# Kernel tuning notes

Measured on AMD Instinct MI355X. Metric: run time of the kernel, lower is better.

## Reference

```python
import jax, jax.numpy as jnp
import numpy as np

D_MODEL = 1024
D_STATE = 16
D_CONV = 4
EXPAND = 2
D_INNER = EXPAND * D_MODEL          # 2048
DT_RANK = D_INNER // 16             # 128
BATCH = 2
SEQLEN = 1024


def _silu(x):
    return x * jax.nn.sigmoid(x)


def setup_inputs() -> dict:
    key = jax.random.key(0)
    ks = jax.random.split(key, 8)
    s = 0.02
    A_init = jnp.tile(jnp.arange(1, D_STATE + 1, dtype=jnp.float32)[None, :], (D_INNER, 1))
    return {
        "x": jax.random.normal(ks[0], (BATCH, SEQLEN, D_MODEL), jnp.float32),
        "W_in": jax.random.normal(ks[1], (D_MODEL, 2 * D_INNER), jnp.float32) * s,
        "conv_k": jax.random.normal(ks[2], (D_CONV, 1, D_INNER), jnp.float32) * s,  # (kw, in/groups, out)
        "conv_b": jnp.zeros((D_INNER,), jnp.float32),
        "W_xproj": jax.random.normal(ks[3], (D_INNER, DT_RANK + 2 * D_STATE), jnp.float32) * s,
        "W_dt": jax.random.normal(ks[4], (DT_RANK, D_INNER), jnp.float32) * s,
        "b_dt": jnp.zeros((D_INNER,), jnp.float32),
        "A_log": jnp.log(A_init),
        "D": jnp.ones((D_INNER,), jnp.float32),
        "W_out": jax.random.normal(ks[5], (D_INNER, D_MODEL), jnp.float32) * s,
    }


def reference(x, W_in, conv_k, conv_b, W_xproj, W_dt, b_dt, A_log, D, W_out):
    # in_proj and gate split
    xz = x @ W_in                                   # (B, L, 2*Di)
    x_in, z = jnp.split(xz, 2, axis=-1)             # each (B, L, Di)

    # depthwise causal conv1d: left-pad by d_conv-1 (keras padding='causal')
    xp = jnp.pad(x_in, ((0, 0), (D_CONV - 1, 0), (0, 0)))
    x_in = jax.lax.conv_general_dilated(
        xp, conv_k, window_strides=(1,), padding='VALID',
        dimension_numbers=('NWC', 'WIO', 'NWC'),
        feature_group_count=D_INNER) + conv_b
    u = _silu(x_in)                                 # (B, L, Di)

    # input-dependent SSM params
    x_dbl = u @ W_xproj                             # (B, L, dt_rank + 2*N)
    dt_low, Bm, Cm = jnp.split(x_dbl, [DT_RANK, DT_RANK + D_STATE], axis=-1)
    dt = jax.nn.softplus(dt_low @ W_dt + b_dt)      # (B, L, Di)
    A = -jnp.exp(A_log)                             # (Di, N)
    dA = jnp.exp(jnp.einsum('bld,dn->bldn', dt, A)) # (B, L, Di, N)
    dB = jnp.einsum('bld,bln->bldn', dt, Bm)        # (B, L, Di, N)

    # selective scan over sequence length
    def step(h, e):
        a_t, b_t, u_t, c_t = e                      # (B,Di,N), (B,Di,N), (B,Di), (B,N)
        h = a_t * h + b_t * u_t[..., None]
        y_t = jnp.einsum('bdn,bn->bd', h, c_t)
        return h, y_t

    h0 = jnp.zeros((x.shape[0], D_INNER, D_STATE), dtype=x.dtype)
    xs = (jnp.swapaxes(dA, 0, 1), jnp.swapaxes(dB, 0, 1),
          jnp.swapaxes(u, 0, 1), jnp.swapaxes(Cm, 0, 1))
    _, yT = jax.lax.scan(step, h0, xs)              # (L, B, Di)
    y = jnp.swapaxes(yT, 0, 1) + u * D              # skip connection

    return (y * _silu(z)) @ W_out                   # (B, L, d_model)
```

## Files before the change

kernel.cpp:

```cpp
#include <hip/hip_runtime.h>
#include <hip/hip_bf16.h>

#define D_MODEL 1024
#define D_STATE 16
#define D_CONV 4
#define D_INNER 2048
#define DT_RANK 128
#define BATCH 2
#define SEQLEN 1024
#define XCOLS 160
#define NCHUNK 32
#define LCHUNK 32

typedef __hip_bfloat16 bf16;
typedef __attribute__((ext_vector_type(8))) short short8;
typedef __attribute__((ext_vector_type(4))) float f32x4;

__device__ __forceinline__ unsigned short f2bf_bits(float f) {
    bf16 h = __float2bfloat16(f);
    return *(unsigned short*)&h;
}

__device__ __forceinline__ float softplus_f(float x) {
    return fmaxf(x, 0.f) + __logf(1.f + __expf(-fabsf(x)));
}

__device__ __forceinline__ float silu_f(float x) {
    return x / (1.f + __expf(-x));
}

__device__ __forceinline__ void load16_lds(void* lds, const void* g) {
    __builtin_amdgcn_global_load_lds(
        (const __attribute__((address_space(1))) unsigned int*)g,
        (__attribute__((address_space(3))) unsigned int*)lds, 16, 0, 0);
}

__device__ __forceinline__ void transpose_tile(const float* __restrict__ B,
                                               bf16* __restrict__ Bt,
                                               int K, int N, int nt, int kt,
                                               float (*t)[33], int tid)
{
    const int tx = tid & 31, ty = tid >> 5;
    const int n0 = nt * 32, k0 = kt * 32;
    #pragma unroll
    for (int r = 0; r < 4; ++r) {
        int n = n0 + tx;
        t[ty + r * 8][tx] = (n < N) ? B[(size_t)(k0 + ty + r * 8) * N + n] : 0.f;
    }
    __syncthreads();
    #pragma unroll
    for (int r = 0; r < 4; ++r)
        Bt[(size_t)(n0 + ty + r * 8) * K + k0 + tx] = __float2bfloat16(t[tx][ty + r * 8]);
}

__global__ __launch_bounds__(256)
void prep_kernel(const float* __restrict__ x, bf16* __restrict__ x_bf,
                 const float* __restrict__ W_in, bf16* __restrict__ Win_t,
                 const float* __restrict__ W_xproj, bf16* __restrict__ Wxp_t,
                 const float* __restrict__ W_dt, bf16* __restrict__ Wdt_t,
                 const float* __restrict__ W_out, bf16* __restrict__ Wout_t,
                 const float* __restrict__ A_log, float* __restrict__ Aneg)
{
    __shared__ float t[32][33];
    const int tid = threadIdx.x;
    int blk = blockIdx.x;
    if (blk < 4096) {
        transpose_tile(W_in, Win_t, D_MODEL, 2 * D_INNER, blk & 127, blk >> 7, t, tid);
        return;
    }
    blk -= 4096;
    if (blk < 512) {
        transpose_tile(W_xproj, Wxp_t, D_INNER, XCOLS, blk & 7, blk >> 3, t, tid);
        return;
    }
    blk -= 512;
    if (blk < 256) {
        transpose_tile(W_dt, Wdt_t, DT_RANK, D_INNER, blk & 63, blk >> 6, t, tid);
        return;
    }
    blk -= 256;
    if (blk < 2048) {
        transpose_tile(W_out, Wout_t, D_INNER, D_MODEL, blk & 31, blk >> 5, t, tid);
        return;
    }
    blk -= 2048;
    if (blk < 2048) {
        int i = blk * 256 + tid;
        float4 v = ((const float4*)x)[i];
        ushort4 p;
        p.x = f2bf_bits(v.x); p.y = f2bf_bits(v.y);
        p.z = f2bf_bits(v.z); p.w = f2bf_bits(v.w);
        ((ushort4*)x_bf)[i] = p;
        return;
    }
    blk -= 2048;
    {
        int i = blk * 256 + tid;
        Aneg[i] = -__expf(A_log[i]);
    }
}

template<int BN, int EPI>
__global__ __launch_bounds__(256)
void gemm_mfma(const bf16* __restrict__ A, const bf16* __restrict__ Bt,
               float* __restrict__ C, bf16* __restrict__ Cb,
               const float* __restrict__ bias,
               int M, int N, int K, int ldc, int kchunk)
{
    constexpr int WN = (BN == 128) ? 64 : 32;
    constexpr int NJ = WN / 16;
    __shared__ short As[128 * 32];
    __shared__ short Bs[BN * 32];
    const int tid = threadIdx.x;
    const int lane = tid & 63, wave = tid >> 6;
    const int wm = (wave >> 1) * 64, wn = (wave & 1) * WN;
    const int row0 = blockIdx.y * 128, col0 = blockIdx.x * BN;
    const int r_m = lane & 15, r_q = lane >> 4;
    const int kstart = blockIdx.z * kchunk;
    float* Cz = C + (size_t)blockIdx.z * M * ldc;

    const int srow = tid >> 2, schk = (tid & 3) * 8;
    const bf16* Ag0 = A  + (size_t)(row0 + srow)      * K + kstart + schk;
    const bf16* Ag1 = A  + (size_t)(row0 + srow + 64) * K + kstart + schk;
    const bf16* Bg0 = Bt + (size_t)(col0 + srow)      * K + kstart + schk;
    const bf16* Bg1 = Bt + (size_t)(col0 + srow + 64) * K + kstart + schk;
    short* AsW0 = &As[8 * tid];
    short* AsW1 = &As[8 * tid + 2048];
    short* BsW0 = &Bs[8 * tid];
    short* BsW1 = &Bs[8 * tid + 2048];

    f32x4 acc[4][NJ];
    #pragma unroll
    for (int i = 0; i < 4; ++i)
        #pragma unroll
        for (int j = 0; j < NJ; ++j)
            #pragma unroll
            for (int r = 0; r < 4; ++r) acc[i][j][r] = 0.f;

    for (int k0 = 0; k0 < kchunk; k0 += 32) {
        __syncthreads();
        load16_lds(AsW0, Ag0 + k0);
        load16_lds(AsW1, Ag1 + k0);
        load16_lds(BsW0, Bg0 + k0);
        if (BN == 128) load16_lds(BsW1, Bg1 + k0);
        __syncthreads();
        short8 af[4], bfr[NJ];
        #pragma unroll
        for (int i = 0; i < 4; ++i)
            af[i] = *(const short8*)&As[(wm + i * 16 + r_m) * 32 + r_q * 8];
        #pragma unroll
        for (int j = 0; j < NJ; ++j)
            bfr[j] = *(const short8*)&Bs[(wn + j * 16 + r_m) * 32 + r_q * 8];
        #pragma unroll
        for (int i = 0; i < 4; ++i)
            #pragma unroll
            for (int j = 0; j < NJ; ++j)
                acc[i][j] = __builtin_amdgcn_mfma_f32_16x16x32_bf16(
                    af[i], bfr[j], acc[i][j], 0, 0, 0);
    }

    #pragma unroll
    for (int i = 0; i < 4; ++i) {
        #pragma unroll
        for (int j = 0; j < NJ; ++j) {
            int row = row0 + wm + i * 16 + r_q * 4;
            int col = col0 + wn + j * 16 + r_m;
            if (col < N) {
                if (EPI == 1) {
                    float bv = bias[col];
                    #pragma unroll
                    for (int r = 0; r < 4; ++r)
                        Cb[(size_t)(row + r) * ldc + col] =
                            __float2bfloat16(softplus_f(acc[i][j][r] + bv));
                } else if (EPI == 2) {
                    if (col < 2048) {
                        #pragma unroll
                        for (int r = 0; r < 4; ++r)
                            Cz[(size_t)(row + r) * ldc + col] = acc[i][j][r];
                    } else {
                        int zc = col - 2048;
                        #pragma unroll
                        for (int r = 0; r < 4; ++r)
                            Cb[(size_t)(row + r) * ldc + zc] =
                                __float2bfloat16(silu_f(acc[i][j][r]));
                    }
                } else {
                    #pragma unroll
                    for (int r = 0; r < 4; ++r)
                        Cz[(size_t)(row + r) * ldc + col] = acc[i][j][r];
                }
            }
        }
    }
}

__global__ __launch_bounds__(256)
void reduce_xdbl(const float* __restrict__ Cpart, float* __restrict__ x_dbl,
                 bf16* __restrict__ dtA_bf)
{
    int i = blockIdx.x * 256 + threadIdx.x;
    if (i >= 2048 * XCOLS) return;
    int r = i / XCOLS, c = i - r * XCOLS;
    float s = 0.f;
    #pragma unroll
    for (int z = 0; z < 8; ++z)
        s += Cpart[(size_t)z * 2048 * 256 + (size_t)r * 256 + c];
    x_dbl[i] = s;
    if (c < DT_RANK) dtA_bf[(size_t)r * DT_RANK + c] = __float2bfloat16(s);
}

__global__ __launch_bounds__(256)
void reduce_out(const float* __restrict__ Cpart, float* __restrict__ out)
{
    int i = blockIdx.x * 256 + threadIdx.x;
    const size_t stride = (size_t)2048 * 1024 / 4;
    const float4* p = (const float4*)Cpart;
    float4 a = p[i], b = p[i + stride], c = p[i + 2 * stride], d = p[i + 3 * stride];
    float4 r;
    r.x = (a.x + b.x) + (c.x + d.x);
    r.y = (a.y + b.y) + (c.y + d.y);
    r.z = (a.z + b.z) + (c.z + d.z);
    r.w = (a.w + b.w) + (c.w + d.w);
    ((float4*)out)[i] = r;
}

__global__ __launch_bounds__(256)
void conv_silu_kernel(const float* __restrict__ x_lin,
                      const float* __restrict__ conv_k,
                      const float* __restrict__ conv_b,
                      bf16* __restrict__ u_bf)
{
    int idx4 = blockIdx.x * 256 + threadIdx.x;
    int d4 = idx4 & (D_INNER / 4 - 1);
    int t = (idx4 >> 9) & (SEQLEN - 1);
    int b = idx4 >> 19;
    float4 acc = ((const float4*)conv_b)[d4];
    #pragma unroll
    for (int k = 0; k < D_CONV; ++k) {
        int tt = t + k - (D_CONV - 1);
        if (tt >= 0) {
            float4 xv = ((const float4*)x_lin)[(size_t)(b * SEQLEN + tt) * (D_INNER / 4) + d4];
            float4 kv = ((const float4*)conv_k)[k * (D_INNER / 4) + d4];
            acc.x = fmaf(xv.x, kv.x, acc.x);
            acc.y = fmaf(xv.y, kv.y, acc.y);
            acc.z = fmaf(xv.z, kv.z, acc.z);
            acc.w = fmaf(xv.w, kv.w, acc.w);
        }
    }
    ushort4 pk;
    pk.x = f2bf_bits(acc.x / (1.f + __expf(-acc.x)));
    pk.y = f2bf_bits(acc.y / (1.f + __expf(-acc.y)));
    pk.z = f2bf_bits(acc.z / (1.f + __expf(-acc.z)));
    pk.w = f2bf_bits(acc.w / (1.f + __expf(-acc.w)));
    ((ushort4*)u_bf)[idx4] = pk;
}

__global__ __launch_bounds__(256)
void scan_phase1(const bf16* __restrict__ dt_sb,
                 const float* __restrict__ Aneg,
                 const bf16* __restrict__ u_bf,
                 const float* __restrict__ x_dbl,
                 float* __restrict__ Pst, float* __restrict__ Sst)
{
    __shared__ float Bsm[LCHUNK][16];
    const int d = blockIdx.x * 256 + threadIdx.x;
    const int c = blockIdx.y, b = blockIdx.z;
    const int t0 = c * LCHUNK;
    for (int i = threadIdx.x; i < LCHUNK * 16; i += 256) {
        int tt = i >> 4, n = i & 15;
        Bsm[tt][n] = x_dbl[(size_t)(b * SEQLEN + t0 + tt) * XCOLS + DT_RANK + n];
    }
    float A_row[D_STATE];
    const float4* a4 = (const float4*)(Aneg + d * D_STATE);
    #pragma unroll
    for (int q = 0; q < 4; ++q) {
        float4 v = a4[q];
        A_row[q*4+0] = v.x; A_row[q*4+1] = v.y; A_row[q*4+2] = v.z; A_row[q*4+3] = v.w;
    }
    __syncthreads();
    float P[D_STATE], S[D_STATE];
    #pragma unroll
    for (int n = 0; n < D_STATE; ++n) { P[n] = 1.f; S[n] = 0.f; }
    const bf16* dpp = dt_sb + (size_t)(b * SEQLEN + t0) * D_INNER + d;
    const bf16* upp = u_bf + (size_t)(b * SEQLEN + t0) * D_INNER + d;
    #pragma unroll 8
    for (int t = 0; t < LCHUNK; ++t) {
        float dtv = __bfloat162float(dpp[(size_t)t * D_INNER]);
        float du = dtv * __bfloat162float(upp[(size_t)t * D_INNER]);
        const float4* b4 = (const float4*)&Bsm[t][0];
        #pragma unroll
        for (int q = 0; q < 4; ++q) {
            float4 v = b4[q];
            float Bn[4] = {v.x, v.y, v.z, v.w};
            #pragma unroll
            for (int e = 0; e < 4; ++e) {
                int n = q * 4 + e;
                float a = __expf(dtv * A_row[n]);
                P[n] *= a;
                S[n] = fmaf(a, S[n], du * Bn[e]);
            }
        }
    }
    const size_t base = ((size_t)(b * NCHUNK + c) * D_STATE) * D_INNER + d;
    #pragma unroll
    for (int n = 0; n < D_STATE; ++n) {
        Pst[base + (size_t)n * D_INNER] = P[n];
        Sst[base + (size_t)n * D_INNER] = S[n];
    }
}

__global__ __launch_bounds__(256)
void scan_phase2(const float* __restrict__ Pst, float* __restrict__ Sst)
{
    const int d = blockIdx.x * 256 + threadIdx.x;
    const int n = blockIdx.y;
    const int b = blockIdx.z;
    float h = 0.f;
    for (int c = 0; c < NCHUNK; ++c) {
        const size_t idx = ((size_t)(b * NCHUNK + c) * D_STATE + n) * D_INNER + d;
        float Pv = Pst[idx], Sv = Sst[idx];
        Sst[idx] = h;
        h = fmaf(Pv, h, Sv);
    }
}

__global__ __launch_bounds__(256)
void scan_phase3(const bf16* __restrict__ dt_sb,
                 const float* __restrict__ Aneg,
                 const bf16* __restrict__ u_bf,
                 const float* __restrict__ x_dbl,
                 const float* __restrict__ Dvec,
                 const bf16* __restrict__ sz_bf,
                 const float* __restrict__ hin,
                 bf16* __restrict__ g_bf)
{
    __shared__ float BCs[LCHUNK][32];
    const int d = blockIdx.x * 256 + threadIdx.x;
    const int c = blockIdx.y, b = blockIdx.z;
    const int t0 = c * LCHUNK;
    for (int i = threadIdx.x; i < LCHUNK * 32; i += 256) {
        int tt = i >> 5, col = i & 31;
        BCs[tt][col] = x_dbl[(size_t)(b * SEQLEN + t0 + tt) * XCOLS + DT_RANK + col];
    }
    float A_row[D_STATE];
    const float4* a4 = (const float4*)(Aneg + d * D_STATE);
    #pragma unroll
    for (int q = 0; q < 4; ++q) {
        float4 v = a4[q];
        A_row[q*4+0] = v.x; A_row[q*4+1] = v.y; A_row[q*4+2] = v.z; A_row[q*4+3] = v.w;
    }
    const float Dd = Dvec[d];
    __syncthreads();
    float h[D_STATE];
    const size_t base = ((size_t)(b * NCHUNK + c) * D_STATE) * D_INNER + d;
    #pragma unroll
    for (int n = 0; n < D_STATE; ++n) h[n] = hin[base + (size_t)n * D_INNER];
    const bf16* dpp = dt_sb + (size_t)(b * SEQLEN + t0) * D_INNER + d;
    const bf16* upp = u_bf + (size_t)(b * SEQLEN + t0) * D_INNER + d;
    const bf16* zpp = sz_bf + (size_t)(b * SEQLEN + t0) * D_INNER + d;
    bf16* gpp = g_bf + (size_t)(b * SEQLEN + t0) * D_INNER + d;
    #pragma unroll 8
    for (int t = 0; t < LCHUNK; ++t) {
        float dtv = __bfloat162float(dpp[(size_t)t * D_INNER]);
        float uv = __bfloat162float(upp[(size_t)t * D_INNER]);
        float sz = __bfloat162float(zpp[(size_t)t * D_INNER]);
        float du = dtv * uv;
        float y = 0.f;
        const float4* bc4 = (const float4*)&BCs[t][0];
        #pragma unroll
        for (int q = 0; q < 4; ++q) {
            float4 v = bc4[q];
            float4 w = bc4[q + 4];
            float Bn[4] = {v.x, v.y, v.z, v.w};
            float Cn[4] = {w.x, w.y, w.z, w.w};
            #pragma unroll
            for (int e = 0; e < 4; ++e) {
                int n = q * 4 + e;
                float a = __expf(dtv * A_row[n]);
                h[n] = fmaf(a, h[n], du * Bn[e]);
                y = fmaf(h[n], Cn[e], y);
            }
        }
        float gy = y + uv * Dd;
        gpp[(size_t)t * D_INNER] = __float2bfloat16(gy * sz);
    }
}

extern "C" void kernel_launch(void* const* d_in, const int* in_sizes, int n_in,
                              void* d_out, int out_size, void* d_ws, size_t ws_size,
                              hipStream_t stream)
{
    const float* x      = (const float*)d_in[0];
    const float* W_in   = (const float*)d_in[1];
    const float* conv_k = (const float*)d_in[2];
    const float* conv_b = (const float*)d_in[3];
    const float* W_xproj= (const float*)d_in[4];
    const float* W_dt   = (const float*)d_in[5];
    const float* b_dt   = (const float*)d_in[6];
    const float* A_log  = (const float*)d_in[7];
    const float* Dvec   = (const float*)d_in[8];
    const float* W_out  = (const float*)d_in[9];
    float* out = (float*)d_out;

    const int BL = BATCH * SEQLEN;

    float* ws     = (float*)d_ws;
    float* x_lin  = ws;
    float* x_dbl  = x_lin + (size_t)BL * D_INNER;
    float* Pst    = x_dbl + (size_t)BL * XCOLS;
    float* Sst    = Pst + (size_t)BATCH * NCHUNK * D_STATE * D_INNER;
    float* Aneg   = Sst + (size_t)BATCH * NCHUNK * D_STATE * D_INNER;
    float* Cpart  = Aneg + 32768;
    bf16*  x_bf   = (bf16*)Cpart;
    bf16* Win_t  = (bf16*)(Cpart + (size_t)4 * 2048 * 1024);
    bf16* u_bf   = Win_t + (size_t)4096 * 1024;
    bf16* sz_bf  = u_bf  + (size_t)BL * D_INNER;
    bf16* Wxp_t  = sz_bf + (size_t)BL * D_INNER;
    bf16* dtA_bf = Wxp_t + (size_t)256 * 2048;
    bf16* Wdt_t  = dtA_bf+ (size_t)BL * DT_RANK;
    bf16* g_bf   = Wdt_t + (size_t)2048 * 128;
    bf16* Wout_t = g_bf  + (size_t)BL * D_INNER;
    bf16* dt_sb  = Wout_t+ (size_t)1024 * 2048;

    prep_kernel<<<4096 + 512 + 256 + 2048 + 2048 + 128, 256, 0, stream>>>(
        x, x_bf, W_in, Win_t, W_xproj, Wxp_t, W_dt, Wdt_t, W_out, Wout_t, A_log, Aneg);

    gemm_mfma<128, 2><<<dim3(32, 16, 1), 256, 0, stream>>>(
        x_bf, Win_t, x_lin, sz_bf, nullptr, BL, 2 * D_INNER, D_MODEL, D_INNER, D_MODEL);

    conv_silu_kernel<<<(BL * D_INNER / 4) / 256, 256, 0, stream>>>(x_lin, conv_k, conv_b, u_bf);

    gemm_mfma<64, 0><<<dim3(3, 16, 8), 256, 0, stream>>>(
        u_bf, Wxp_t, Cpart, nullptr, nullptr, BL, 256, D_INNER, 256, 256);
    reduce_xdbl<<<(BL * XCOLS + 255) / 256, 256, 0, stream>>>(Cpart, x_dbl, dtA_bf);

    gemm_mfma<64, 1><<<dim3(32, 16, 1), 256, 0, stream>>>(
        dtA_bf, Wdt_t, nullptr, dt_sb, b_dt, BL, D_INNER, DT_RANK, D_INNER, DT_RANK);

    scan_phase1<<<dim3(D_INNER / 256, NCHUNK, BATCH), 256, 0, stream>>>(
        dt_sb, Aneg, u_bf, x_dbl, Pst, Sst);
    scan_phase2<<<dim3(D_INNER / 256, D_STATE, BATCH), 256, 0, stream>>>(Pst, Sst);
    scan_phase3<<<dim3(D_INNER / 256, NCHUNK, BATCH), 256, 0, stream>>>(
        dt_sb, Aneg, u_bf, x_dbl, Dvec, sz_bf, Sst, g_bf);

    gemm_mfma<128, 0><<<dim3(8, 16, 4), 256, 0, stream>>>(
        g_bf, Wout_t, Cpart, nullptr, nullptr, BL, D_MODEL, D_INNER, D_MODEL, D_INNER / 4);
    reduce_out<<<(BL * D_MODEL / 4) / 256, 256, 0, stream>>>(Cpart, out);
}
```

Before: 255.7 us.

## Store in-proj x as bf16, vectorize conv and reductions, retile out-proj split-K

The in-projection GEMM now writes the conv input half as bf16 rather than fp32. The conv kernel reads it 8 elements at a time, which halves that traffic. reduce_xdbl is vectorized to float4. The output GEMM moves from BN=128 with 4-way split-K to BN=64 with 2-way split-K, which halves the partial-sum traffic in reduce_out. Scan loop unroll drops from 8 to 4. Rounding the pre-conv activations to bf16 adds some precision loss.

```diff
diff --git a/kernel.cpp b/kernel.cpp
--- a/kernel.cpp
+++ b/kernel.cpp
@@ -21,6 +21,12 @@
     return *(unsigned short*)&h;
 }
 
+__device__ __forceinline__ float bfbits2f(short s) {
+    union { float f; unsigned u; } v;
+    v.u = ((unsigned)(unsigned short)s) << 16;
+    return v.f;
+}
+
 __device__ __forceinline__ float softplus_f(float x) {
     return fmaxf(x, 0.f) + __logf(1.f + __expf(-fabsf(x)));
 }
@@ -104,6 +110,7 @@
 __global__ __launch_bounds__(256)
 void gemm_mfma(const bf16* __restrict__ A, const bf16* __restrict__ Bt,
                float* __restrict__ C, bf16* __restrict__ Cb,
+               bf16* __restrict__ Cb2,
                const float* __restrict__ bias,
                int M, int N, int K, int ldc, int kchunk)
 {
@@ -176,7 +183,8 @@
                     if (col < 2048) {
                         #pragma unroll
                         for (int r = 0; r < 4; ++r)
-                            Cz[(size_t)(row + r) * ldc + col] = acc[i][j][r];
+                            Cb2[(size_t)(row + r) * ldc + col] =
+                                __float2bfloat16(acc[i][j][r]);
                     } else {
                         int zc = col - 2048;
                         #pragma unroll
@@ -198,61 +206,74 @@
 void reduce_xdbl(const float* __restrict__ Cpart, float* __restrict__ x_dbl,
                  bf16* __restrict__ dtA_bf)
 {
+    int i4 = blockIdx.x * 256 + threadIdx.x;
+    if (i4 >= 2048 * (XCOLS / 4)) return;
+    int r = i4 / (XCOLS / 4), c4 = i4 - r * (XCOLS / 4);
+    float4 s = {0.f, 0.f, 0.f, 0.f};
+    #pragma unroll
+    for (int z = 0; z < 8; ++z) {
+        float4 v = *(const float4*)&Cpart[(size_t)z * 2048 * 256 + (size_t)r * 256 + c4 * 4];
+        s.x += v.x; s.y += v.y; s.z += v.z; s.w += v.w;
+    }
+    *(float4*)&x_dbl[(size_t)r * XCOLS + c4 * 4] = s;
+    if (c4 < DT_RANK / 4) {
+        ushort4 p;
+        p.x = f2bf_bits(s.x); p.y = f2bf_bits(s.y);
+        p.z = f2bf_bits(s.z); p.w = f2bf_bits(s.w);
+        *(ushort4*)&dtA_bf[(size_t)r * DT_RANK + c4 * 4] = p;
+    }
+}
+
+__global__ __launch_bounds__(256)
+void reduce_out(const float* __restrict__ Cpart, float* __restrict__ out)
+{
     int i = blockIdx.x * 256 + threadIdx.x;
-    if (i >= 2048 * XCOLS) return;
-    int r = i / XCOLS, c = i - r * XCOLS;
-    float s = 0.f;
-    #pragma unroll
-    for (int z = 0; z < 8; ++z)
-        s += Cpart[(size_t)z * 2048 * 256 + (size_t)r * 256 + c];
-    x_dbl[i] = s;
-    if (c < DT_RANK) dtA_bf[(size_t)r * DT_RANK + c] = __float2bfloat16(s);
-}
-
-__global__ __launch_bounds__(256)
-void reduce_out(const float* __restrict__ Cpart, float* __restrict__ out)
-{
-    int i = blockIdx.x * 256 + threadIdx.x;
-    const size_t stride = (size_t)2048 * 1024 / 4;
-    const float4* p = (const float4*)Cpart;
-    float4 a = p[i], b = p[i + stride], c = p[i + 2 * stride], d = p[i + 3 * stride];
-    float4 r;
-    r.x = (a.x + b.x) + (c.x + d.x);
-    r.y = (a.y + b.y) + (c.y + d.y);
-    r.z = (a.z + b.z) + (c.z + d.z);
-    r.w = (a.w + b.w) + (c.w + d.w);
+    const float4* p0 = (const float4*)Cpart;
+    const float4* p1 = p0 + (size_t)2048 * 1024 / 4;
+    float4 a = p0[i], b = p1[i];
+    float4 r; r.x = a.x + b.x; r.y = a.y + b.y; r.z = a.z + b.z; r.w = a.w + b.w;
     ((float4*)out)[i] = r;
 }
 
 __global__ __launch_bounds__(256)
-void conv_silu_kernel(const float* __restrict__ x_lin,
+void conv_silu_kernel(const bf16* __restrict__ xd,
                       const float* __restrict__ conv_k,
                       const float* __restrict__ conv_b,
                       bf16* __restrict__ u_bf)
 {
-    int idx4 = blockIdx.x * 256 + threadIdx.x;
-    int d4 = idx4 & (D_INNER / 4 - 1);
-    int t = (idx4 >> 9) & (SEQLEN - 1);
-    int b = idx4 >> 19;
-    float4 acc = ((const float4*)conv_b)[d4];
+    int idx8 = blockIdx.x * 256 + threadIdx.x;
+    int d8 = idx8 & (D_INNER / 8 - 1);
+    int t = (idx8 >> 8) & (SEQLEN - 1);
+    int b = idx8 >> 18;
+    float acc[8];
+    {
+        float4 b0 = ((const float4*)conv_b)[d8 * 2];
+        float4 b1 = ((const float4*)conv_b)[d8 * 2 + 1];
+        acc[0] = b0.x; acc[1] = b0.y; acc[2] = b0.z; acc[3] = b0.w;
+        acc[4] = b1.x; acc[5] = b1.y; acc[6] = b1.z; acc[7] = b1.w;
+    }
     #pragma unroll
     for (int k = 0; k < D_CONV; ++k) {
         int tt = t + k - (D_CONV - 1);
         if (tt >= 0) {
-            float4 xv = ((const float4*)x_lin)[(size_t)(b * SEQLEN + tt) * (D_INNER / 4) + d4];
-            float4 kv = ((const float4*)conv_k)[k * (D_INNER / 4) + d4];
-            acc.x = fmaf(xv.x, kv.x, acc.x);
-            acc.y = fmaf(xv.y, kv.y, acc.y);
-            acc.z = fmaf(xv.z, kv.z, acc.z);
-            acc.w = fmaf(xv.w, kv.w, acc.w);
+            short8 xv = ((const short8*)xd)[(size_t)(b * SEQLEN + tt) * (D_INNER / 8) + d8];
+            float4 k0 = ((const float4*)conv_k)[k * (D_INNER / 4) + d8 * 2];
+            float4 k1 = ((const float4*)conv_k)[k * (D_INNER / 4) + d8 * 2 + 1];
+            acc[0] = fmaf(bfbits2f(xv[0]), k0.x, acc[0]);
+            acc[1] = fmaf(bfbits2f(xv[1]), k0.y, acc[1]);
+            acc[2] = fmaf(bfbits2f(xv[2]), k0.z, acc[2]);
+            acc[3] = fmaf(bfbits2f(xv[3]), k0.w, acc[3]);
+            acc[4] = fmaf(bfbits2f(xv[4]), k1.x, acc[4]);
+            acc[5] = fmaf(bfbits2f(xv[5]), k1.y, acc[5]);
+            acc[6] = fmaf(bfbits2f(xv[6]), k1.z, acc[6]);
+            acc[7] = fmaf(bfbits2f(xv[7]), k1.w, acc[7]);
         }
     }
-    ushort4 pk;
-    pk.x = f2bf_bits(acc.x / (1.f + __expf(-acc.x)));
-    pk.y = f2bf_bits(acc.y / (1.f + __expf(-acc.y)));
-    pk.z = f2bf_bits(acc.z / (1.f + __expf(-acc.z)));
-    pk.w = f2bf_bits(acc.w / (1.f + __expf(-acc.w)));
-    ((ushort4*)u_bf)[idx4] = pk;
+    short8 r;
+    #pragma unroll
+    for (int j = 0; j < 8; ++j)
+        r[j] = (short)f2bf_bits(acc[j] / (1.f + __expf(-acc[j])));
+    ((short8*)u_bf)[idx8] = r;
 }
 
 __global__ __launch_bounds__(256)
@@ -283,7 +304,7 @@
     for (int n = 0; n < D_STATE; ++n) { P[n] = 1.f; S[n] = 0.f; }
     const bf16* dpp = dt_sb + (size_t)(b * SEQLEN + t0) * D_INNER + d;
     const bf16* upp = u_bf + (size_t)(b * SEQLEN + t0) * D_INNER + d;
-    #pragma unroll 8
+    #pragma unroll 4
     for (int t = 0; t < LCHUNK; ++t) {
         float dtv = __bfloat162float(dpp[(size_t)t * D_INNER]);
         float du = dtv * __bfloat162float(upp[(size_t)t * D_INNER]);
@@ -359,7 +380,7 @@
     const bf16* upp = u_bf + (size_t)(b * SEQLEN + t0) * D_INNER + d;
     const bf16* zpp = sz_bf + (size_t)(b * SEQLEN + t0) * D_INNER + d;
     bf16* gpp = g_bf + (size_t)(b * SEQLEN + t0) * D_INNER + d;
-    #pragma unroll 8
+    #pragma unroll 4
     for (int t = 0; t < LCHUNK; ++t) {
         float dtv = __bfloat162float(dpp[(size_t)t * D_INNER]);
         float uv = __bfloat162float(upp[(size_t)t * D_INNER]);
@@ -405,15 +426,15 @@
     const int BL = BATCH * SEQLEN;
 
     float* ws     = (float*)d_ws;
-    float* x_lin  = ws;
-    float* x_dbl  = x_lin + (size_t)BL * D_INNER;
+    float* x_dbl  = ws;
     float* Pst    = x_dbl + (size_t)BL * XCOLS;
     float* Sst    = Pst + (size_t)BATCH * NCHUNK * D_STATE * D_INNER;
     float* Aneg   = Sst + (size_t)BATCH * NCHUNK * D_STATE * D_INNER;
     float* Cpart  = Aneg + 32768;
     bf16*  x_bf   = (bf16*)Cpart;
-    bf16* Win_t  = (bf16*)(Cpart + (size_t)4 * 2048 * 1024);
-    bf16* u_bf   = Win_t + (size_t)4096 * 1024;
+    bf16* Win_t  = (bf16*)(Cpart + (size_t)4 * 1048576);
+    bf16* xd_bf  = Win_t + (size_t)4096 * 1024;
+    bf16* u_bf   = xd_bf + (size_t)BL * D_INNER;
     bf16* sz_bf  = u_bf  + (size_t)BL * D_INNER;
     bf16* Wxp_t  = sz_bf + (size_t)BL * D_INNER;
     bf16* dtA_bf = Wxp_t + (size_t)256 * 2048;
@@ -426,16 +447,16 @@
         x, x_bf, W_in, Win_t, W_xproj, Wxp_t, W_dt, Wdt_t, W_out, Wout_t, A_log, Aneg);
 
     gemm_mfma<128, 2><<<dim3(32, 16, 1), 256, 0, stream>>>(
-        x_bf, Win_t, x_lin, sz_bf, nullptr, BL, 2 * D_INNER, D_MODEL, D_INNER, D_MODEL);
-
-    conv_silu_kernel<<<(BL * D_INNER / 4) / 256, 256, 0, stream>>>(x_lin, conv_k, conv_b, u_bf);
+        x_bf, Win_t, nullptr, sz_bf, xd_bf, nullptr, BL, 2 * D_INNER, D_MODEL, D_INNER, D_MODEL);
+
+    conv_silu_kernel<<<(BL * D_INNER / 8) / 256, 256, 0, stream>>>(xd_bf, conv_k, conv_b, u_bf);
 
     gemm_mfma<64, 0><<<dim3(3, 16, 8), 256, 0, stream>>>(
-        u_bf, Wxp_t, Cpart, nullptr, nullptr, BL, 256, D_INNER, 256, 256);
-    reduce_xdbl<<<(BL * XCOLS + 255) / 256, 256, 0, stream>>>(Cpart, x_dbl, dtA_bf);
+        u_bf, Wxp_t, Cpart, nullptr, nullptr, nullptr, BL, 256, D_INNER, 256, 256);
+    reduce_xdbl<<<(BL * (XCOLS / 4) + 255) / 256, 256, 0, stream>>>(Cpart, x_dbl, dtA_bf);
 
     gemm_mfma<64, 1><<<dim3(32, 16, 1), 256, 0, stream>>>(
-        dtA_bf, Wdt_t, nullptr, dt_sb, b_dt, BL, D_INNER, DT_RANK, D_INNER, DT_RANK);
+        dtA_bf, Wdt_t, nullptr, dt_sb, nullptr, b_dt, BL, D_INNER, DT_RANK, D_INNER, DT_RANK);
 
     scan_phase1<<<dim3(D_INNER / 256, NCHUNK, BATCH), 256, 0, stream>>>(
         dt_sb, Aneg, u_bf, x_dbl, Pst, Sst);
@@ -443,7 +464,7 @@
     scan_phase3<<<dim3(D_INNER / 256, NCHUNK, BATCH), 256, 0, stream>>>(
         dt_sb, Aneg, u_bf, x_dbl, Dvec, sz_bf, Sst, g_bf);
 
-    gemm_mfma<128, 0><<<dim3(8, 16, 4), 256, 0, stream>>>(
-        g_bf, Wout_t, Cpart, nullptr, nullptr, BL, D_MODEL, D_INNER, D_MODEL, D_INNER / 4);
+    gemm_mfma<64, 0><<<dim3(16, 16, 2), 256, 0, stream>>>(
+        g_bf, Wout_t, Cpart, nullptr, nullptr, nullptr, BL, D_MODEL, D_INNER, D_MODEL, D_INNER / 2);
     reduce_out<<<(BL * D_MODEL / 4) / 256, 256, 0, stream>>>(Cpart, out);
 }
```

Measured after the change: 237.6 us. 1.08x faster.
